# Kernel optimization log

Hardware: AMD Instinct MI355X
Metric: run time of the kernel (lower is better)

## Reference

```python
import jax, jax.numpy as jnp
import numpy as np


def setup_inputs() -> dict:
    key = jax.random.key(0)
    k1, k2, k3 = jax.random.split(key, 3)
    # N=5 pyramid-level node features, each [B=1, C=256, H=64, W=64]
    x = jax.random.normal(k1, (5, 1, 256, 64, 64), dtype=jnp.float32)
    # Conv2d(512, 256, kernel_size=1) == per-pixel linear; stored as [in=512, out=256]
    conv_w = jax.random.normal(k2, (512, 256), dtype=jnp.float32) * 0.04
    conv_b = jax.random.normal(k3, (256,), dtype=jnp.float32) * 0.01
    return {"x": x, "conv_w": conv_w, "conv_b": conv_b}


def reference(x, conv_w, conv_b):
    # x: [N, B, C, H, W] stacked node features
    N, B, C, H, W = x.shape
    pixels = B * C * H * W
    THRESH = 0.35

    # Vectorized pairwise score (original double python loop over (i, j)):
    # make_score(x_i, x_j): target = conv1x1(cat([x_j, x_i + x_j])); |x_j - target|
    xi = x[:, None]                      # [N,1,B,C,H,W]
    xj = x[None, :]                      # [1,N,B,C,H,W]
    x_add = xi + xj                      # [N,N,B,C,H,W]
    xj_b = jnp.broadcast_to(xj, x_add.shape)
    cat = jnp.concatenate([xj_b, x_add], axis=3)          # [N,N,B,2C,H,W]
    # 1x1 conv == channel contraction
    target = jnp.einsum('ijbchw,cd->ijbdhw', cat, conv_w) \
        + conv_b[None, None, None, :, None, None]          # [N,N,B,C,H,W]
    dist = jnp.abs(xj_b - target)                          # [N,N,B,C,H,W]

    # edge_list[:, i, j] = dist(i, j) flattened over (B,C,H,W)
    edge = dist.reshape(N, N, pixels).transpose(2, 0, 1)   # [pixels, N, N]

    # node matrix: [pixels, N, 1]
    node = x.reshape(N, pixels).T[..., None]

    # F.normalize(p=2, dim=2) then keep ORIGINAL values where normalized > t
    norm = jnp.sqrt(jnp.sum(edge * edge, axis=2, keepdims=True))
    edge_n = edge / jnp.maximum(norm, 1e-12)
    edge_t = jnp.where(edge_n > THRESH, edge, jnp.zeros((), dtype=edge.dtype))

    # feat_fusion: [pixels,N,N] @ [pixels,N,1] -> [pixels,N] -> [N,pixels]
    h = (edge_t @ node)[..., 0].T                          # [N, pixels]
    out = h.reshape(N, B, C, H, W)
    return out
```

## Files before the change

### kernel.cpp

```cpp
#include <hip/hip_runtime.h>
#include <math.h>

constexpr int NIMG = 5;
constexpr int CCH  = 256;
constexpr int HWP  = 4096;
constexpr int PT   = CCH * HWP;

constexpr int BD = 32;
constexpr int BP = 64;
constexpr int BK = 16;
constexpr int NSTEP = CCH / BK;

__device__ __forceinline__ void gload16(const float* g, float* l) {
    __builtin_amdgcn_global_load_lds(
        (const __attribute__((address_space(1))) unsigned int*)g,
        (__attribute__((address_space(3))) unsigned int*)l, 16, 0, 0);
}

__global__ __launch_bounds__(256, 2) void fused_all(
    const float* __restrict__ x, const float* __restrict__ w,
    const float* __restrict__ bias, float* __restrict__ out)
{
    const int t  = threadIdx.x;
    const int tp = t & 15;
    const int td = t >> 4;
    const int p0 = blockIdx.x * BP;
    const int d0 = blockIdx.y * BD;

    __shared__ float xs [2][NIMG][BK][BP];
    __shared__ float w1s[2][BK][BD];
    __shared__ float w2s[2][BK][BD];

    float acc_s[NIMG][2][4] = {};
    float acc_2[NIMG][2][4] = {};

    const int wv = t >> 6, l = t & 63;
    const int xr = l >> 4, xc = (l & 15) * 4;
    const int wr = l >> 3, wc = (l & 7) * 4;

    auto stage = [&](int b, int c0) {
        #pragma unroll
        for (int s = 0; s < NIMG; ++s) {
            const int g = wv + 4 * s;
            const int n = g >> 2, k = g & 3;
            gload16(&x[(size_t)n * PT + (size_t)(c0 + k * 4 + xr) * HWP + p0 + xc],
                    &xs[b][n][k * 4][0]);
        }
        if (wv < 2) {
            gload16(&w[(size_t)(c0 + wv * 8 + wr) * CCH + d0 + wc],
                    &w1s[b][wv * 8][0]);
        } else {
            gload16(&w[(size_t)(256 + c0 + (wv - 2) * 8 + wr) * CCH + d0 + wc],
                    &w2s[b][(wv - 2) * 8][0]);
        }
    };

    stage(0, 0);

    for (int st = 0; st < NSTEP; ++st) {
        const int cur = st & 1;
        if (st + 1 < NSTEP) {
            stage(cur ^ 1, (st + 1) * BK);
            asm volatile("s_waitcnt vmcnt(6)" ::: "memory");
        } else {
            asm volatile("s_waitcnt vmcnt(0)" ::: "memory");
        }
        __builtin_amdgcn_s_barrier();

        #pragma unroll
        for (int cc = 0; cc < BK; ++cc) {
            const float2 w1v = *reinterpret_cast<const float2*>(&w1s[cur][cc][td * 2]);
            const float2 w2v = *reinterpret_cast<const float2*>(&w2s[cur][cc][td * 2]);
            const float w2a[2] = {w2v.x, w2v.y};
            const float wsa[2] = {w1v.x + w2v.x, w1v.y + w2v.y};
            #pragma unroll
            for (int n = 0; n < NIMG; ++n) {
                const float4 xv = *reinterpret_cast<const float4*>(&xs[cur][n][cc][tp * 4]);
                const float xa[4] = {xv.x, xv.y, xv.z, xv.w};
                #pragma unroll
                for (int i = 0; i < 2; ++i) {
                    #pragma unroll
                    for (int j = 0; j < 4; ++j) {
                        acc_s[n][i][j] = fmaf(wsa[i], xa[j], acc_s[n][i][j]);
                        acc_2[n][i][j] = fmaf(w2a[i], xa[j], acc_2[n][i][j]);
                    }
                }
            }
        }
        __builtin_amdgcn_s_barrier();
    }

    #pragma unroll
    for (int r = 0; r < 2; ++r) {
        const int d = d0 + td * 2 + r;
        const float bd = bias[d];
        const size_t base = (size_t)d * HWP + p0 + tp * 4;

        float xa[NIMG][4], ua[NIMG][4], va[NIMG][4];
        #pragma unroll
        for (int n = 0; n < NIMG; ++n) {
            const float4 xv = *reinterpret_cast<const float4*>(&x[(size_t)n * PT + base]);
            const float xt[4] = {xv.x, xv.y, xv.z, xv.w};
            #pragma unroll
            for (int q = 0; q < 4; ++q) {
                xa[n][q] = xt[q];
                ua[n][q] = xt[q] - acc_s[n][r][q] - bd;
                va[n][q] = acc_2[n][r][q];
            }
        }

        #pragma unroll
        for (int i = 0; i < NIMG; ++i) {
            float ho[4];
            #pragma unroll
            for (int q = 0; q < 4; ++q) {
                float e[NIMG];
                float sumsq = 0.0f;
                #pragma unroll
                for (int j = 0; j < NIMG; ++j) {
                    e[j] = fabsf(ua[j][q] - va[i][q]);
                    sumsq = fmaf(e[j], e[j], sumsq);
                }
                const float m = fmaxf(sqrtf(sumsq), 1e-12f);
                float h = 0.0f;
                #pragma unroll
                for (int j = 0; j < NIMG; ++j) {
                    const float en = e[j] / m;
                    if (en > 0.35f) h = fmaf(e[j], xa[j][q], h);
                }
                ho[q] = h;
            }
            const float4 ov = {ho[0], ho[1], ho[2], ho[3]};
            *reinterpret_cast<float4*>(&out[(size_t)i * PT + base]) = ov;
        }
    }
}

extern "C" void kernel_launch(void* const* d_in, const int* in_sizes, int n_in,
                              void* d_out, int out_size, void* d_ws, size_t ws_size,
                              hipStream_t stream) {
    const float* x    = (const float*)d_in[0];
    const float* w    = (const float*)d_in[1];
    const float* bias = (const float*)d_in[2];
    float* out = (float*)d_out;

    dim3 g(HWP / BP, CCH / BD);
    fused_all<<<g, 256, 0, stream>>>(x, w, bias, out);
}
```

Baseline: 82.83 us.

## Reshape block tile to 64 outputs by 32 pixels with rebalanced LDS staging

```diff
diff --git a/kernel.cpp b/kernel.cpp
--- a/kernel.cpp
+++ b/kernel.cpp
@@ -6,8 +6,8 @@
 constexpr int HWP  = 4096;
 constexpr int PT   = CCH * HWP;
 
-constexpr int BD = 32;
-constexpr int BP = 64;
+constexpr int BD = 64;
+constexpr int BP = 32;
 constexpr int BK = 16;
 constexpr int NSTEP = CCH / BK;
 
@@ -31,27 +31,32 @@
     __shared__ float w1s[2][BK][BD];
     __shared__ float w2s[2][BK][BD];
 
-    float acc_s[NIMG][2][4] = {};
-    float acc_2[NIMG][2][4] = {};
+    float acc_s[NIMG][4][2] = {};
+    float acc_2[NIMG][4][2] = {};
 
     const int wv = t >> 6, l = t & 63;
-    const int xr = l >> 4, xc = (l & 15) * 4;
-    const int wr = l >> 3, wc = (l & 7) * 4;
+    const int xr = l >> 3, xc = (l & 7) * 4;
+    const int wr = l >> 4, wc = (l & 15) * 4;
 
     auto stage = [&](int b, int c0) {
-        #pragma unroll
-        for (int s = 0; s < NIMG; ++s) {
-            const int g = wv + 4 * s;
-            const int n = g >> 2, k = g & 3;
-            gload16(&x[(size_t)n * PT + (size_t)(c0 + k * 4 + xr) * HWP + p0 + xc],
-                    &xs[b][n][k * 4][0]);
-        }
         if (wv < 2) {
-            gload16(&w[(size_t)(c0 + wv * 8 + wr) * CCH + d0 + wc],
-                    &w1s[b][wv * 8][0]);
+            #pragma unroll
+            for (int s = 0; s < 5; ++s) {
+                const int g = wv * 5 + s;
+                const int n = g >> 1, half = g & 1;
+                gload16(&x[(size_t)n * PT + (size_t)(c0 + half * 8 + xr) * HWP + p0 + xc],
+                        &xs[b][n][half * 8][0]);
+            }
+        } else if (wv == 2) {
+            #pragma unroll
+            for (int k = 0; k < 4; ++k)
+                gload16(&w[(size_t)(c0 + k * 4 + wr) * CCH + d0 + wc],
+                        &w1s[b][k * 4][0]);
         } else {
-            gload16(&w[(size_t)(256 + c0 + (wv - 2) * 8 + wr) * CCH + d0 + wc],
-                    &w2s[b][(wv - 2) * 8][0]);
+            #pragma unroll
+            for (int k = 0; k < 4; ++k)
+                gload16(&w[(size_t)(256 + c0 + k * 4 + wr) * CCH + d0 + wc],
+                        &w2s[b][k * 4][0]);
         }
     };
 
@@ -61,7 +66,8 @@
         const int cur = st & 1;
         if (st + 1 < NSTEP) {
             stage(cur ^ 1, (st + 1) * BK);
-            asm volatile("s_waitcnt vmcnt(6)" ::: "memory");
+            if (wv < 2) asm volatile("s_waitcnt vmcnt(5)" ::: "memory");
+            else        asm volatile("s_waitcnt vmcnt(4)" ::: "memory");
         } else {
             asm volatile("s_waitcnt vmcnt(0)" ::: "memory");
         }
@@ -69,18 +75,19 @@
 
         #pragma unroll
         for (int cc = 0; cc < BK; ++cc) {
-            const float2 w1v = *reinterpret_cast<const float2*>(&w1s[cur][cc][td * 2]);
-            const float2 w2v = *reinterpret_cast<const float2*>(&w2s[cur][cc][td * 2]);
-            const float w2a[2] = {w2v.x, w2v.y};
-            const float wsa[2] = {w1v.x + w2v.x, w1v.y + w2v.y};
+            const float4 w1v = *reinterpret_cast<const float4*>(&w1s[cur][cc][td * 4]);
+            const float4 w2v = *reinterpret_cast<const float4*>(&w2s[cur][cc][td * 4]);
+            const float w2a[4] = {w2v.x, w2v.y, w2v.z, w2v.w};
+            const float wsa[4] = {w1v.x + w2v.x, w1v.y + w2v.y,
+                                  w1v.z + w2v.z, w1v.w + w2v.w};
             #pragma unroll
             for (int n = 0; n < NIMG; ++n) {
-                const float4 xv = *reinterpret_cast<const float4*>(&xs[cur][n][cc][tp * 4]);
-                const float xa[4] = {xv.x, xv.y, xv.z, xv.w};
+                const float2 xv = *reinterpret_cast<const float2*>(&xs[cur][n][cc][tp * 2]);
+                const float xa[2] = {xv.x, xv.y};
                 #pragma unroll
-                for (int i = 0; i < 2; ++i) {
+                for (int i = 0; i < 4; ++i) {
                     #pragma unroll
-                    for (int j = 0; j < 4; ++j) {
+                    for (int j = 0; j < 2; ++j) {
                         acc_s[n][i][j] = fmaf(wsa[i], xa[j], acc_s[n][i][j]);
                         acc_2[n][i][j] = fmaf(w2a[i], xa[j], acc_2[n][i][j]);
                     }
@@ -91,18 +98,18 @@
     }
 
     #pragma unroll
-    for (int r = 0; r < 2; ++r) {
-        const int d = d0 + td * 2 + r;
+    for (int r = 0; r < 4; ++r) {
+        const int d = d0 + td * 4 + r;
         const float bd = bias[d];
-        const size_t base = (size_t)d * HWP + p0 + tp * 4;
+        const size_t base = (size_t)d * HWP + p0 + tp * 2;
 
-        float xa[NIMG][4], ua[NIMG][4], va[NIMG][4];
+        float xa[NIMG][2], ua[NIMG][2], va[NIMG][2];
         #pragma unroll
         for (int n = 0; n < NIMG; ++n) {
-            const float4 xv = *reinterpret_cast<const float4*>(&x[(size_t)n * PT + base]);
-            const float xt[4] = {xv.x, xv.y, xv.z, xv.w};
+            const float2 xv = *reinterpret_cast<const float2*>(&x[(size_t)n * PT + base]);
+            const float xt[2] = {xv.x, xv.y};
             #pragma unroll
-            for (int q = 0; q < 4; ++q) {
+            for (int q = 0; q < 2; ++q) {
                 xa[n][q] = xt[q];
                 ua[n][q] = xt[q] - acc_s[n][r][q] - bd;
                 va[n][q] = acc_2[n][r][q];
@@ -111,9 +118,9 @@
 
         #pragma unroll
         for (int i = 0; i < NIMG; ++i) {
-            float ho[4];
+            float ho[2];
             #pragma unroll
-            for (int q = 0; q < 4; ++q) {
+            for (int q = 0; q < 2; ++q) {
                 float e[NIMG];
                 float sumsq = 0.0f;
                 #pragma unroll
@@ -130,8 +137,8 @@
                 }
                 ho[q] = h;
             }
-            const float4 ov = {ho[0], ho[1], ho[2], ho[3]};
-            *reinterpret_cast<float4*>(&out[(size_t)i * PT + base]) = ov;
+            const float2 ov = {ho[0], ho[1]};
+            *reinterpret_cast<float2*>(&out[(size_t)i * PT + base]) = ov;
         }
     }
 }
```

Result: slower. 86.38 us (+4.3%).

## Retile GEMM so each wave owns 4 output channels with wave-uniform weight loads

Applied to the files above, without the earlier changes.

```diff
diff --git a/kernel.cpp b/kernel.cpp
--- a/kernel.cpp
+++ b/kernel.cpp
@@ -6,9 +6,7 @@
 constexpr int HWP  = 4096;
 constexpr int PT   = CCH * HWP;
 
-constexpr int BD = 32;
-constexpr int BP = 64;
-constexpr int BK = 16;
+constexpr int BK = 8;
 constexpr int NSTEP = CCH / BK;
 
 __device__ __forceinline__ void gload16(const float* g, float* l) {
@@ -21,37 +19,24 @@
     const float* __restrict__ x, const float* __restrict__ w,
     const float* __restrict__ bias, float* __restrict__ out)
 {
-    const int t  = threadIdx.x;
-    const int tp = t & 15;
-    const int td = t >> 4;
-    const int p0 = blockIdx.x * BP;
-    const int d0 = blockIdx.y * BD;
+    const int lane = threadIdx.x & 63;
+    const int wv   = __builtin_amdgcn_readfirstlane(threadIdx.x >> 6);
+    const int d0w  = blockIdx.x * 16 + wv * 4;
+    const int p0   = blockIdx.y * 256;
+    const int pl   = p0 + lane * 4;
 
-    __shared__ float xs [2][NIMG][BK][BP];
-    __shared__ float w1s[2][BK][BD];
-    __shared__ float w2s[2][BK][BD];
+    __shared__ float xs[2][NIMG][BK][256];
 
-    float acc_s[NIMG][2][4] = {};
-    float acc_2[NIMG][2][4] = {};
-
-    const int wv = t >> 6, l = t & 63;
-    const int xr = l >> 4, xc = (l & 15) * 4;
-    const int wr = l >> 3, wc = (l & 7) * 4;
+    float acc_s[NIMG][4][4] = {};
+    float acc_2[NIMG][4][4] = {};
 
     auto stage = [&](int b, int c0) {
         #pragma unroll
-        for (int s = 0; s < NIMG; ++s) {
-            const int g = wv + 4 * s;
-            const int n = g >> 2, k = g & 3;
-            gload16(&x[(size_t)n * PT + (size_t)(c0 + k * 4 + xr) * HWP + p0 + xc],
-                    &xs[b][n][k * 4][0]);
-        }
-        if (wv < 2) {
-            gload16(&w[(size_t)(c0 + wv * 8 + wr) * CCH + d0 + wc],
-                    &w1s[b][wv * 8][0]);
-        } else {
-            gload16(&w[(size_t)(256 + c0 + (wv - 2) * 8 + wr) * CCH + d0 + wc],
-                    &w2s[b][(wv - 2) * 8][0]);
+        for (int k = 0; k < 10; ++k) {
+            const int rho = wv + 4 * k;
+            const int n = rho >> 3, cc = rho & 7;
+            gload16(&x[(size_t)n * PT + (size_t)(c0 + cc) * HWP + p0 + lane * 4],
+                    &xs[b][n][cc][0]);
         }
     };
 
@@ -61,7 +46,7 @@
         const int cur = st & 1;
         if (st + 1 < NSTEP) {
             stage(cur ^ 1, (st + 1) * BK);
-            asm volatile("s_waitcnt vmcnt(6)" ::: "memory");
+            asm volatile("s_waitcnt vmcnt(10)" ::: "memory");
         } else {
             asm volatile("s_waitcnt vmcnt(0)" ::: "memory");
         }
@@ -69,20 +54,25 @@
 
         #pragma unroll
         for (int cc = 0; cc < BK; ++cc) {
-            const float2 w1v = *reinterpret_cast<const float2*>(&w1s[cur][cc][td * 2]);
-            const float2 w2v = *reinterpret_cast<const float2*>(&w2s[cur][cc][td * 2]);
-            const float w2a[2] = {w2v.x, w2v.y};
-            const float wsa[2] = {w1v.x + w2v.x, w1v.y + w2v.y};
+            const int c = st * BK + cc;
+            const float4 w1v = *reinterpret_cast<const float4*>(
+                &w[(size_t)c * CCH + d0w]);
+            const float4 w2v = *reinterpret_cast<const float4*>(
+                &w[(size_t)(CCH + c) * CCH + d0w]);
+            const float w2a[4] = {w2v.x, w2v.y, w2v.z, w2v.w};
+            const float wsa[4] = {w1v.x + w2v.x, w1v.y + w2v.y,
+                                  w1v.z + w2v.z, w1v.w + w2v.w};
             #pragma unroll
             for (int n = 0; n < NIMG; ++n) {
-                const float4 xv = *reinterpret_cast<const float4*>(&xs[cur][n][cc][tp * 4]);
+                const float4 xv = *reinterpret_cast<const float4*>(
+                    &xs[cur][n][cc][lane * 4]);
                 const float xa[4] = {xv.x, xv.y, xv.z, xv.w};
                 #pragma unroll
-                for (int i = 0; i < 2; ++i) {
+                for (int r = 0; r < 4; ++r) {
                     #pragma unroll
-                    for (int j = 0; j < 4; ++j) {
-                        acc_s[n][i][j] = fmaf(wsa[i], xa[j], acc_s[n][i][j]);
-                        acc_2[n][i][j] = fmaf(w2a[i], xa[j], acc_2[n][i][j]);
+                    for (int q = 0; q < 4; ++q) {
+                        acc_s[n][r][q] = fmaf(wsa[r], xa[q], acc_s[n][r][q]);
+                        acc_2[n][r][q] = fmaf(w2a[r], xa[q], acc_2[n][r][q]);
                     }
                 }
             }
@@ -91,10 +81,10 @@
     }
 
     #pragma unroll
-    for (int r = 0; r < 2; ++r) {
-        const int d = d0 + td * 2 + r;
+    for (int r = 0; r < 4; ++r) {
+        const int d = d0w + r;
         const float bd = bias[d];
-        const size_t base = (size_t)d * HWP + p0 + tp * 4;
+        const size_t base = (size_t)d * HWP + pl;
 
         float xa[NIMG][4], ua[NIMG][4], va[NIMG][4];
         #pragma unroll
@@ -144,6 +134,6 @@
     const float* bias = (const float*)d_in[2];
     float* out = (float*)d_out;
 
-    dim3 g(HWP / BP, CCH / BD);
+    dim3 g(CCH / 16, HWP / 256);
     fused_all<<<g, 256, 0, stream>>>(x, w, bias, out);
 }
```

New measurement: 178.2 us. 2.15x slower.
